# Kernel optimization log

Hardware: AMD Instinct MI355X
Metric: run time of the kernel (lower is better)

Reference implementation:

```python
import jax, jax.numpy as jnp
import numpy as np

L = 8192   # sequence length
B = 4      # batch
D = 512    # embed_dim
NDIM = 16  # EMA state dim
Z = 128    # shared q/k dim
W = 128    # attention window
MP = 256   # max relative positions
NEG = -50000.0  # TOKEN_SELF_ATTN_VALUE-style mask fill


def setup_inputs() -> dict:
    key = jax.random.key(0)
    ks = jax.random.split(key, 16)
    def tn(k, shp, std):  # truncated-normal-ish init (clipped normal)
        return jnp.clip(jax.random.normal(k, shp) * std, -2 * std, 2 * std)
    val = jnp.ones((NDIM, 1)).at[1::2].set(-1.0)  # MultiHeadEMA beta init pattern
    return {
        "x": jax.random.normal(ks[0], (L, B, D), dtype=jnp.float32),
        "delta": tn(ks[1], (D, NDIM, 1), 0.2),
        "alpha": tn(ks[2], (D, NDIM, 1), 0.2),
        "beta": tn(ks[3], (D, NDIM, 1), 0.02) + val,
        "gamma": jax.random.normal(ks[4], (D, NDIM)),
        "omega": jax.random.normal(ks[5], (D,)),
        "Wp": tn(ks[6], (D, 1), 0.02),      # LatentConfigurator weight_proj
        "bp": jnp.zeros((1,)),
        "temp": jnp.array([0.5 * np.log(D)], dtype=jnp.float32),  # log(sqrt(D))
        "Wz": tn(ks[7], (D, Z), 0.02),
        "qg": jax.random.normal(ks[8], (Z,)) * 0.02 + 1.0,
        "qb": jnp.zeros((Z,)),
        "kg": jax.random.normal(ks[9], (Z,)) * 0.02 + 1.0,
        "kb": jnp.zeros((Z,)),
        "Wv": tn(ks[10], (D, D), 0.02),
        "relb": tn(ks[11], (2 * MP - 1,), 0.02),  # FastRelativePositionalBias table
    }


def _rotary(t, cos, sin):
    # t: (B, L, Z); cos/sin: (L, Z//2). Complex rotation on interleaved pairs.
    t1, t2 = t[..., 0::2], t[..., 1::2]
    return jnp.stack([t1 * cos - t2 * sin, t1 * sin + t2 * cos], axis=-1).reshape(t.shape)


def _forward(x, delta, alpha, beta, gamma, omega, Wp, bp, temp, Wz, qg, qb, kg, kb, Wv, relb):
    scale = 1.0 / np.sqrt(NDIM)
    # ---- MultiHeadEMA: damped EMA as long convolution via FFT ----
    p = jax.nn.sigmoid(delta)                      # (D,N,1)
    a = jax.nn.sigmoid(alpha)
    logq = jnp.log1p(-(p * a))                     # log(1 - p*alpha)
    t = jnp.arange(L, dtype=jnp.float32)
    kern = (p * beta) * jnp.exp(logq * t)          # (D,N,L) Vandermonde kernel
    k1d = jnp.einsum('dnl,dn->dl', kern, gamma * scale)  # (D,L)
    xb = x.transpose(1, 2, 0)                      # (B,D,L)
    conv = jnp.fft.irfft(jnp.fft.rfft(xb, n=2 * L) * jnp.fft.rfft(k1d, n=2 * L), n=2 * L)[..., :L]
    mx = jax.nn.silu(conv.transpose(2, 0, 1) + x * omega)  # (L,B,D)
    # ---- LatentConfigurator: sigmoid token routing (proj_dim==1) ----
    pi = jax.nn.sigmoid((mx @ Wp + bp) / jnp.exp(temp))[..., 0].T  # (B,L)
    mxb = mx.transpose(1, 0, 2)                    # (B,L,D)
    sel = pi > 0.5
    idx = jnp.cumsum(sel.astype(jnp.int32), axis=1) * sel  # (B,L); 0 -> dropped slot
    counts = sel.sum(axis=1)                       # (B,)
    bi = jnp.arange(B)[:, None]
    # compress_seq: scatter selected tokens to compact prefix (slot 0 dropped)
    c = jnp.zeros((B, L + 1, D), mx.dtype).at[bi, idx].add(mxb * sel[..., None])[:, 1:]
    # ---- windowed attention over compressed tokens ----
    z = jax.nn.silu(c @ Wz)                        # (B,L,Z)
    freqs = 1.0 / (10000.0 ** (jnp.arange(0, Z, 2, dtype=jnp.float32) / Z))
    ang = jnp.arange(L, dtype=jnp.float32)[:, None] * freqs
    cos, sin = jnp.cos(ang), jnp.sin(ang)
    q = _rotary(z * qg + qb, cos, sin)
    kk = _rotary(z * kg + kb, cos, sin)
    v = jax.nn.silu(c @ Wv)                        # (B,L,D)
    n = L // W
    qw = q.reshape(B, n, W, Z)
    def look_around(tw):  # prepend previous window: (B,n,W,f) -> (B,n,2W,f)
        prev = jnp.pad(tw, ((0, 0), (1, 0), (0, 0), (0, 0)))[:, :-1]
        return jnp.concatenate([prev, tw], axis=2)
    kw = look_around(kk.reshape(B, n, W, Z))
    vw = look_around(v.reshape(B, n, W, D))
    base = (jnp.arange(n) * W)[:, None, None]
    qabs = base + jnp.arange(W)[None, :, None]         # (n,W,1)
    kabs = base + jnp.arange(-W, W)[None, None, :]     # (n,1,2W)
    mask = (kabs <= qabs) & (kabs >= 0) & (kabs[None] < counts[:, None, None, None])  # (B,n,W,2W)
    rel = jnp.arange(-W, W)[None, :] - jnp.arange(W)[:, None]   # (W,2W)
    bias = relb[jnp.clip(rel + MP - 1, 0, 2 * MP - 2)]          # (W,2W)
    scores = jnp.einsum('bnwz,bnkz->bnwk', qw, kw) / np.sqrt(Z) + bias
    attn = jax.nn.softmax(jnp.where(mask, scores, NEG), axis=-1)
    h = jnp.einsum('bnwk,bnkd->bnwd', attn, vw).reshape(B, L, D)
    # ---- extract: gather back to original positions, gate by pi ----
    hpad = jnp.concatenate([jnp.zeros((B, 1, D), h.dtype), h], axis=1)
    hsel = jnp.take_along_axis(hpad, idx[..., None], axis=1)    # (B,L,D)
    return x + (hsel * pi[..., None]).transpose(1, 0, 2)        # (L,B,D)


def reference(x, delta, alpha, beta, gamma, omega, Wp, bp, temp, Wz, qg, qb, kg, kb, Wv, relb):
    return _forward(x, delta, alpha, beta, gamma, omega, Wp, bp, temp, Wz, qg, qb, kg, kb, Wv, relb)
```

## Files before the change

### kernel.cpp

```cpp
#include <hip/hip_runtime.h>
#include <math.h>

constexpr int L = 8192;
constexpr int B = 4;
constexpr int D = 512;
constexpr int NDIM = 16;
constexpr int Z = 128;
constexpr float NEGF = -50000.0f;
constexpr int CCL = 32;
constexpr int NCH = L / CCL;
constexpr int FMAX = 64;

typedef short s16x8 __attribute__((ext_vector_type(8)));
typedef float f32x4 __attribute__((ext_vector_type(4)));

typedef __attribute__((address_space(1))) const void* as1cv;
typedef __attribute__((address_space(3))) void* as3v;

__device__ __forceinline__ void gld16(const void* g, void* l) {
  __builtin_amdgcn_global_load_lds((as1cv)g, (as3v)l, 16, 0, 0);
}

__device__ __forceinline__ unsigned short f2bf(float f) {
  unsigned u = __builtin_bit_cast(unsigned, f);
  u += 0x7fffu + ((u >> 16) & 1u);
  return (unsigned short)(u >> 16);
}

#define DPPADD(acc, ctrl, rmask)                                                   \
  {                                                                                \
    int _mv = __builtin_amdgcn_update_dpp(0, __builtin_bit_cast(int, acc),         \
                                          ctrl, rmask, 0xf, false);                \
    acc += __builtin_bit_cast(float, _mv);                                         \
  }

__global__ __launch_bounds__(256) void k_prep(const float* __restrict__ delta,
                                              const float* __restrict__ alpha,
                                              const float* __restrict__ beta,
                                              const float* __restrict__ gamma,
                                              double* __restrict__ qdn,
                                              double* __restrict__ cdn,
                                              double* __restrict__ rp1,
                                              double* __restrict__ rp2,
                                              float* __restrict__ qf,
                                              float* __restrict__ cf,
                                              float* __restrict__ r1f,
                                              float* __restrict__ r2f,
                                              float* __restrict__ r3f,
                                              int* __restrict__ fcnt) {
  int i = blockIdx.x * 256 + threadIdx.x;
  if (i == 0) *fcnt = 0;
  if (i >= D * NDIM) return;
  double p = 1.0 / (1.0 + exp(-(double)delta[i]));
  double a = 1.0 / (1.0 + exp(-(double)alpha[i]));
  double q = 1.0 - p * a;
  double c = p * (double)beta[i] * (double)gamma[i] * 0.25;
  qdn[i] = q; cdn[i] = c;
  double q2 = q * q, q4 = q2 * q2, q8 = q4 * q4;
  double q16 = q8 * q8, q32 = q16 * q16, q64 = q32 * q32;
  rp1[i] = q64;
  rp2[i] = q64 * q64;
  qf[i] = (float)q; cf[i] = (float)c;
  r1f[i] = (float)q32;
  r2f[i] = (float)q64;
  r3f[i] = (float)(q64 * q32);
}

__global__ __launch_bounds__(256) void k_tab(float2* __restrict__ tab) {
  int tid = blockIdx.x * 256 + threadIdx.x;
  int i = tid & 63, j = tid >> 6;
  float freq = __expf(((float)(-2 * i) / 128.0f) * 9.210340371976184f);
  float angf = (float)j * freq;
  float sa, ca;
  __sincosf(angf, &sa, &ca);
  float2 r; r.x = ca; r.y = sa;
  tab[tid] = r;
}

__global__ __launch_bounds__(256, 4) void k_convA(const float* __restrict__ x,
                                                  const float* __restrict__ qf,
                                                  float* __restrict__ E) {
  int bx = blockIdx.x;
  int tile = bx & 63, dg = (bx >> 6) & 7, b = bx >> 9;
  int dl = threadIdx.x & 63, cl = threadIdx.x >> 6;
  int dgl = dg * 64 + dl;
  int t = tile * 4 + cl;
  float q[NDIM], s[NDIM];
#pragma unroll
  for (int n = 0; n < NDIM; ++n) { q[n] = qf[dgl * NDIM + n]; s[n] = 0.f; }
  const float* xp = x + ((size_t)(t * CCL) * B + b) * D + dgl;
  float xv[CCL];
#pragma unroll
  for (int u = 0; u < CCL; ++u) xv[u] = xp[u * (B * D)];
#pragma unroll
  for (int u = 0; u < CCL; ++u) {
#pragma unroll
    for (int n = 0; n < NDIM; ++n) s[n] = fmaf(q[n], s[n], xv[u]);
  }
  float* eb = E + ((size_t)(b * NCH + t) * NDIM) * 512 + dgl;
#pragma unroll
  for (int n = 0; n < NDIM; ++n) eb[(size_t)n * 512] = s[n];
}

__global__ __launch_bounds__(256, 4) void k_convC(const float* __restrict__ x,
                                                  const float* __restrict__ omega,
                                                  const float* __restrict__ qf,
                                                  const float* __restrict__ cf,
                                                  const float* __restrict__ r1f,
                                                  const float* __restrict__ r2f,
                                                  const float* __restrict__ r3f,
                                                  const float* __restrict__ E,
                                                  const float* __restrict__ Wp,
                                                  unsigned short* __restrict__ mxb,
                                                  float* __restrict__ pdot) {
  int bx = blockIdx.x;
  int tile = bx & 63, dg = (bx >> 6) & 7, b = bx >> 9;
  int dl = threadIdx.x & 63, cl = threadIdx.x >> 6;
  int dgl = dg * 64 + dl;
  int t = tile * 4 + cl;
  float q[NDIM], c[NDIM], s[NDIM];
#pragma unroll
  for (int n = 0; n < NDIM; ++n) {
    q[n] = qf[dgl * NDIM + n];
    c[n] = cf[dgl * NDIM + n];
    s[n] = 0.f;
  }
  if (t >= 1) {
    const float* e1 = E + ((size_t)(b * NCH + t - 1) * NDIM) * 512 + dgl;
#pragma unroll
    for (int n = 0; n < NDIM; ++n) s[n] = e1[(size_t)n * 512];
  }
  if (t >= 2) {
    const float* e2 = E + ((size_t)(b * NCH + t - 2) * NDIM) * 512 + dgl;
#pragma unroll
    for (int n = 0; n < NDIM; ++n) s[n] = fmaf(r1f[dgl * NDIM + n], e2[(size_t)n * 512], s[n]);
  }
  if (t >= 3) {
    const float* e3 = E + ((size_t)(b * NCH + t - 3) * NDIM) * 512 + dgl;
#pragma unroll
    for (int n = 0; n < NDIM; ++n) s[n] = fmaf(r2f[dgl * NDIM + n], e3[(size_t)n * 512], s[n]);
  }
  if (t >= 4) {
    const float* e4 = E + ((size_t)(b * NCH + t - 4) * NDIM) * 512 + dgl;
#pragma unroll
    for (int n = 0; n < NDIM; ++n) s[n] = fmaf(r3f[dgl * NDIM + n], e4[(size_t)n * 512], s[n]);
  }
  float om = omega[dgl];
  float wp = Wp[dgl];
  const float* xp = x + ((size_t)(t * CCL) * B + b) * D + dgl;
  unsigned short* mp = mxb + ((size_t)b * L + t * CCL) * 512 + dgl;
  float* pp = pdot + ((size_t)(b * L + t * CCL)) * 8 + dg;
  float xv[CCL];
#pragma unroll
  for (int u = 0; u < CCL; ++u) xv[u] = xp[u * (B * D)];
#pragma unroll
  for (int u = 0; u < CCL; ++u) {
#pragma unroll
    for (int n = 0; n < NDIM; ++n) s[n] = fmaf(q[n], s[n], xv[u]);
    float p0 = c[0] * s[0], p1 = c[1] * s[1], p2 = c[2] * s[2], p3 = c[3] * s[3];
    p0 = fmaf(c[4], s[4], p0);  p1 = fmaf(c[5], s[5], p1);
    p2 = fmaf(c[6], s[6], p2);  p3 = fmaf(c[7], s[7], p3);
    p0 = fmaf(c[8], s[8], p0);  p1 = fmaf(c[9], s[9], p1);
    p2 = fmaf(c[10], s[10], p2); p3 = fmaf(c[11], s[11], p3);
    p0 = fmaf(c[12], s[12], p0); p1 = fmaf(c[13], s[13], p1);
    p2 = fmaf(c[14], s[14], p2); p3 = fmaf(c[15], s[15], p3);
    float conv = (p0 + p1) + (p2 + p3);
    float m = fmaf(xv[u], om, conv);
    float v = m / (1.0f + __expf(-m));
    mp[(size_t)u * 512] = f2bf(v);
    float pd = v * wp;
    DPPADD(pd, 0x111, 0xf);
    DPPADD(pd, 0x112, 0xf);
    DPPADD(pd, 0x114, 0xf);
    DPPADD(pd, 0x118, 0xf);
    DPPADD(pd, 0x142, 0xa);
    DPPADD(pd, 0x143, 0x8);
    if (dl == 63) pp[(size_t)u * 8] = pd;
  }
}

__global__ __launch_bounds__(256) void k_logitc(const float* __restrict__ pdot,
                                                const float* __restrict__ bp,
                                                const float* __restrict__ temp,
                                                float* __restrict__ pi,
                                                int* __restrict__ selb,
                                                int* __restrict__ fcnt,
                                                int* __restrict__ flags) {
  int rid = blockIdx.x * 256 + threadIdx.x;
  const float* pr = pdot + (size_t)rid * 8;
  double acc = 0.0;
#pragma unroll
  for (int j = 0; j < 8; ++j) acc += (double)pr[j];
  double logit = acc + (double)bp[0];
  pi[rid] = (float)(1.0 / (1.0 + exp(-logit / exp((double)temp[0]))));
  selb[rid] = (logit > 0.0) ? 1 : 0;
  if (fabs(logit) < 1e-4) {
    int slot = atomicAdd(fcnt, 1);
    if (slot < FMAX) flags[slot] = rid;
  }
}

__global__ __launch_bounds__(256) void k_fix(const int* __restrict__ fcnt,
                                             const int* __restrict__ flags,
                                             const float* __restrict__ x,
                                             const double* __restrict__ qdn,
                                             const double* __restrict__ cdn,
                                             const double* __restrict__ rp1,
                                             const double* __restrict__ rp2,
                                             const float* __restrict__ omega,
                                             const float* __restrict__ Wp,
                                             double* __restrict__ pfix) {
  int nb = blockIdx.x;
  int fi = nb >> 3, dblk = nb & 7;
  int count = *fcnt; if (count > FMAX) count = FMAX;
  if (fi >= count) return;
  int rid = flags[fi];
  int b = rid >> 13, l = rid & (L - 1);
  int t = l >> 6, io = l & 63;
  int sub = threadIdx.x >> 6, dl = threadIdx.x & 63;
  int d = dblk * 64 + dl;
  double q[NDIM], s[NDIM];
#pragma unroll
  for (int n = 0; n < NDIM; ++n) { q[n] = qdn[d * NDIM + n]; s[n] = 0.0; }
  int c0 = (sub < 3) ? (t - 3 + sub) : t;
  int steps = (sub < 3) ? 64 : (io + 1);
  if (c0 >= 0) {
    const float* xp = x + ((size_t)(c0 * 64) * B + b) * D + d;
    for (int i = 0; i < steps; ++i) {
      double xv = (double)xp[(size_t)i * (B * D)];
#pragma unroll
      for (int n = 0; n < NDIM; ++n) s[n] = fma(q[n], s[n], xv);
    }
  }
  __shared__ double Esm[4][64][NDIM];
#pragma unroll
  for (int n = 0; n < NDIM; ++n) Esm[sub][dl][n] = s[n];
  __syncthreads();
  if (sub == 3) {
    double sfin[NDIM];
#pragma unroll
    for (int n = 0; n < NDIM; ++n) {
      double base = q[n], r = 1.0;
      int e = io + 1;
      while (e) { if (e & 1) r *= base; base *= base; e >>= 1; }
      double S = Esm[2][dl][n] + rp1[d * NDIM + n] * Esm[1][dl][n] + rp2[d * NDIM + n] * Esm[0][dl][n];
      sfin[n] = Esm[3][dl][n] + r * S;
    }
    double conv = 0.0;
#pragma unroll
    for (int n = 0; n < NDIM; ++n) conv = fma(cdn[d * NDIM + n], sfin[n], conv);
    double xv = (double)x[((size_t)l * B + b) * D + d];
    double m = conv + xv * (double)omega[d];
    double mxd = m / (1.0 + exp(-m));
    double v = mxd * (double)Wp[d];
#pragma unroll
    for (int off = 32; off; off >>= 1) v += __shfl_down(v, off, 64);
    if (dl == 0) pfix[fi * 8 + dblk] = v;
  }
}

__global__ __launch_bounds__(64) void k_fix2(const int* __restrict__ fcnt,
                                             const int* __restrict__ flags,
                                             const double* __restrict__ pfix,
                                             const float* __restrict__ bp,
                                             const float* __restrict__ temp,
                                             float* __restrict__ pi,
                                             int* __restrict__ selb) {
  int fi = threadIdx.x;
  int count = *fcnt; if (count > FMAX) count = FMAX;
  if (fi >= count) return;
  double s = 0.0;
#pragma unroll
  for (int j = 0; j < 8; ++j) s += pfix[fi * 8 + j];
  double logit = s + (double)bp[0];
  int rid = flags[fi];
  selb[rid] = (logit > 0.0) ? 1 : 0;
  pi[rid] = (float)(1.0 / (1.0 + exp(-logit / exp((double)temp[0]))));
}

__global__ __launch_bounds__(256) void k_scan(const int* __restrict__ selb,
                                              int* __restrict__ idx,
                                              int* __restrict__ src,
                                              int* __restrict__ counts) {
  int b = blockIdx.x;
  int t = threadIdx.x;
  __shared__ int part[256];
  const int PER = L / 256;
  int base = b * L + t * PER;
  int loc[PER];
  int cnt = 0;
#pragma unroll
  for (int i = 0; i < PER; ++i) { loc[i] = selb[base + i]; cnt += loc[i]; }
  part[t] = cnt;
  __syncthreads();
  for (int off = 1; off < 256; off <<= 1) {
    int v = (t >= off) ? part[t - off] : 0;
    __syncthreads();
    part[t] += v;
    __syncthreads();
  }
  int run = (t == 0) ? 0 : part[t - 1];
#pragma unroll
  for (int i = 0; i < PER; ++i) {
    int sflag = loc[i];
    run += sflag;
    idx[base + i] = sflag ? run : 0;
    if (sflag) src[b * L + run - 1] = t * PER + i;
  }
  if (t == 255) counts[b] = part[255];
  __syncthreads();
  int total = part[255];
  for (int i2 = total + t; i2 < L; i2 += 256) src[b * L + i2] = 0;
}

__global__ __launch_bounds__(256) void k_wt(const float* __restrict__ Wm,
                                            unsigned short* __restrict__ Wt, int N) {
  int idx = blockIdx.x * 256 + threadIdx.x;
  int n = idx >> 9, kk = idx & 511;
  Wt[idx] = f2bf(Wm[(size_t)kk * N + n]);
}

__global__ __launch_bounds__(256) void k_gemm_mfma(const unsigned short* __restrict__ mxb,
                                                   const int* __restrict__ src,
                                                   const int* __restrict__ counts,
                                                   const unsigned short* __restrict__ Bt,
                                                   float* __restrict__ outF,
                                                   unsigned short* __restrict__ outT,
                                                   int N, int mode) {
  __shared__ char smem[32768];
  char* As = smem;
  char* Bs = smem + 16384;
  int tid = threadIdx.x;
  int w = tid >> 6, l = tid & 63;
  int mtile, ntile;
  if (mode == 1) {
    int lin = blockIdx.y * 256 + blockIdx.x;
    int xcd = lin & 7, loc = lin >> 3;
    mtile = xcd * 32 + (loc >> 2);
    ntile = loc & 3;
  } else {
    mtile = blockIdx.x; ntile = blockIdx.y;
  }
  int m0 = mtile * 128, n0 = ntile * 128;
  int gb = m0 >> 13, j0 = m0 & 8191;
  if (j0 >= counts[gb]) return;
  int wr = w >> 1, wc = w & 1;
  const unsigned short* arow[4];
  const unsigned short* brow[4];
#pragma unroll
  for (int ld = 0; ld < 4; ++ld) {
    int li = w * 4 + ld;
    int row = li * 8 + (l >> 3);
    int col = ((l & 7) ^ (row & 7)) << 3;
    int srow = src[gb * 8192 + j0 + row];
    arow[ld] = mxb + ((size_t)gb * 8192 + srow) * 512 + col;
    brow[ld] = Bt + (size_t)(n0 + row) * 512 + col;
  }
  f32x4 acc[4][4];
  f32x4 zz = {0.f, 0.f, 0.f, 0.f};
#pragma unroll
  for (int mi = 0; mi < 4; ++mi)
#pragma unroll
    for (int ni = 0; ni < 4; ++ni) acc[mi][ni] = zz;

  for (int k0 = 0; k0 < 512; k0 += 64) {
#pragma unroll
    for (int ld = 0; ld < 4; ++ld) {
      int li = w * 4 + ld;
      gld16(arow[ld] + k0, As + li * 1024);
      gld16(brow[ld] + k0, Bs + li * 1024);
    }
    __syncthreads();
    s16x8 af[4][2], bfr[4][2];
#pragma unroll
    for (int kh = 0; kh < 2; ++kh) {
#pragma unroll
      for (int mi = 0; mi < 4; ++mi) {
        int row = wr * 64 + mi * 16 + (l & 15);
        int byte = row * 128 + ((kh * 64 + ((l >> 4) * 16)) ^ ((row & 7) << 4));
        af[mi][kh] = *(const s16x8*)(As + byte);
      }
#pragma unroll
      for (int ni = 0; ni < 4; ++ni) {
        int row = wc * 64 + ni * 16 + (l & 15);
        int byte = row * 128 + ((kh * 64 + ((l >> 4) * 16)) ^ ((row & 7) << 4));
        bfr[ni][kh] = *(const s16x8*)(Bs + byte);
      }
    }
#pragma unroll
    for (int kh = 0; kh < 2; ++kh)
#pragma unroll
      for (int mi = 0; mi < 4; ++mi)
#pragma unroll
        for (int ni = 0; ni < 4; ++ni)
          acc[mi][ni] = __builtin_amdgcn_mfma_f32_16x16x32_bf16(af[mi][kh], bfr[ni][kh], acc[mi][ni], 0, 0, 0);
    __syncthreads();
  }
  if (mode == 0) {
#pragma unroll
    for (int mi = 0; mi < 4; ++mi)
#pragma unroll
      for (int ni = 0; ni < 4; ++ni)
#pragma unroll
        for (int r = 0; r < 4; ++r) {
          float vv = acc[mi][ni][r];
          vv = vv / (1.0f + __expf(-vv));
          int mrow = m0 + wr * 64 + mi * 16 + (l >> 4) * 4 + r;
          int ncol = n0 + wc * 64 + ni * 16 + (l & 15);
          outF[(size_t)mrow * N + ncol] = vv;
        }
  } else {
#pragma unroll
    for (int mi = 0; mi < 4; ++mi)
#pragma unroll
      for (int ni = 0; ni < 4; ++ni)
#pragma unroll
        for (int r = 0; r < 4; ++r) {
          float vv = acc[mi][ni][r];
          vv = vv / (1.0f + __expf(-vv));
          int mrow = wr * 64 + mi * 16 + (l >> 4) * 4 + r;
          int ncol = wc * 64 + ni * 16 + (l & 15);
          int byteoff = ncol * 256 + ((mrow * 2) ^ ((ncol & 7) << 4));
          *(unsigned short*)(smem + byteoff) = f2bf(vv);
        }
    __syncthreads();
#pragma unroll
    for (int it = 0; it < 8; ++it) {
      int ncol = w * 32 + it * 4 + (l >> 4);
      int ch = l & 15;
      int byteoff = ncol * 256 + ((ch * 16) ^ ((ncol & 7) << 4));
      s16x8 vch = *(const s16x8*)(smem + byteoff);
      *(s16x8*)(outT + ((size_t)(gb * 512 + n0 + ncol)) * 8192 + j0 + ch * 8) = vch;
    }
  }
}

__global__ __launch_bounds__(256) void k_rot(const float* __restrict__ z,
                                             const float2* __restrict__ tab,
                                             const int* __restrict__ counts,
                                             const float* __restrict__ qg,
                                             const float* __restrict__ qb,
                                             const float* __restrict__ kg,
                                             const float* __restrict__ kb,
                                             unsigned short* __restrict__ qo,
                                             unsigned short* __restrict__ ko) {
  int tid = blockIdx.x * 256 + threadIdx.x;
  int i = tid & 63;
  int row = tid >> 6;
  int j = row & (L - 1);
  int b = row >> 13;
  if (j >= counts[b]) return;
  float2 cs = tab[j * 64 + i];
  float cc = cs.x, ss = cs.y;
  size_t base = (size_t)row * Z + 2 * i;
  float z1 = z[base], z2 = z[base + 1];
  float q1 = z1 * qg[2 * i] + qb[2 * i], q2 = z2 * qg[2 * i + 1] + qb[2 * i + 1];
  float k1 = z1 * kg[2 * i] + kb[2 * i], k2 = z2 * kg[2 * i + 1] + kb[2 * i + 1];
  qo[base]     = f2bf(q1 * cc - q2 * ss);
  qo[base + 1] = f2bf(q1 * ss + q2 * cc);
  ko[base]     = f2bf(k1 * cc - k2 * ss);
  ko[base + 1] = f2bf(k1 * ss + k2 * cc);
}

__global__ __launch_bounds__(256) void k_attn_mfma(const unsigned short* __restrict__ q,
                                                   const unsigned short* __restrict__ k,
                                                   const unsigned short* __restrict__ vT,
                                                   const float* __restrict__ relb,
                                                   const int* __restrict__ counts,
                                                   const int* __restrict__ src,
                                                   const float* __restrict__ pi,
                                                   const float* __restrict__ x,
                                                   float* __restrict__ out) {
  __shared__ char smem[49152];
  char* A  = smem;
  char* Bv = smem + 32768;
  int tid = threadIdx.x, w = tid >> 6, l = tid & 63;
  int bid = blockIdx.x;
  int n = bid >> 3, b = (bid >> 1) & 3, half = bid & 1;
  int cnt = counts[b];
  int q0 = n * 128 + half * 64;
  if (q0 >= cnt) return;
  int kbase = n * 128 - 128;
  const size_t rowb = (size_t)b * L;
  int m0 = w * 16;
  int lg = l >> 4;

  s16x8 aq[4];
  {
    const unsigned short* qrow = q + (rowb + q0 + m0 + (l & 15)) * Z + lg * 8;
#pragma unroll
    for (int ks = 0; ks < 4; ++ks) aq[ks] = *(const s16x8*)(qrow + ks * 32);
  }

  f32x4 s[16];
  f32x4 zz = {0.f, 0.f, 0.f, 0.f};
#pragma unroll
  for (int ni = 0; ni < 16; ++ni) s[ni] = zz;
#pragma unroll
  for (int kh2 = 0; kh2 < 2; ++kh2) {
#pragma unroll
    for (int ld = 0; ld < 8; ++ld) {
      int li = w * 8 + ld;
      int rowl = li * 4 + (l >> 4);
      int jk = kbase + kh2 * 128 + rowl;
      if (jk < 0) jk = 0;
      int colb = ((l & 15) * 16) ^ ((rowl & 7) << 4);
      gld16((const char*)(k + (rowb + jk) * Z) + colb, A + li * 1024);
    }
    __syncthreads();
#pragma unroll
    for (int ni8 = 0; ni8 < 8; ++ni8) {
      int ni = kh2 * 8 + ni8;
      int rowl = ni8 * 16 + (l & 15);
      int rb = rowl * 256, sw = (rowl & 7) << 4;
#pragma unroll
      for (int ks = 0; ks < 4; ++ks) {
        s16x8 bk = *(const s16x8*)(A + rb + ((ks * 64 + lg * 16) ^ sw));
        s[ni] = __builtin_amdgcn_mfma_f32_16x16x32_bf16(aq[ks], bk, s[ni], 0, 0, 0);
      }
    }
    __syncthreads();
  }

  auto stageV = [&](int nc) {
#pragma unroll
    for (int ld = 0; ld < 4; ++ld) {
      int li = w * 4 + ld;
      int row = li * 2 + (l >> 5);
      int colb = ((l & 31) * 16) ^ ((row & 7) << 4);
      int j = kbase + (colb >> 1);
      if (j < 0) j = 0;
      gld16((const char*)(vT + ((size_t)(b * 512 + nc * 32 + row)) * L + j), Bv + li * 1024);
    }
  };
  stageV(0);

  int rgrp = lg * 4;
  float mxr[4] = {-3e38f, -3e38f, -3e38f, -3e38f};
#pragma unroll
  for (int ni = 0; ni < 16; ++ni) {
    int col = ni * 16 + (l & 15);
    int kabs = kbase + col;
#pragma unroll
    for (int r = 0; r < 4; ++r) {
      int ww = half * 64 + m0 + rgrp + r;
      bool valid = (kabs >= 0) && (kabs <= n * 128 + ww) && (kabs < cnt);
      float vv = valid ? (s[ni][r] * 0.08838834764831845f + relb[col + 127 - ww]) : NEGF;
      s[ni][r] = vv;
      mxr[r] = fmaxf(mxr[r], vv);
    }
  }
#pragma unroll
  for (int r = 0; r < 4; ++r)
    for (int off = 1; off < 16; off <<= 1)
      mxr[r] = fmaxf(mxr[r], __shfl_xor(mxr[r], off, 64));
  float smr[4] = {0.f, 0.f, 0.f, 0.f};
#pragma unroll
  for (int ni = 0; ni < 16; ++ni)
#pragma unroll
    for (int r = 0; r < 4; ++r) {
      float p = __expf(s[ni][r] - mxr[r]);
      s[ni][r] = p;
      smr[r] += p;
    }
#pragma unroll
  for (int r = 0; r < 4; ++r) {
    for (int off = 1; off < 16; off <<= 1) smr[r] += __shfl_xor(smr[r], off, 64);
    smr[r] = 1.0f / smr[r];
  }
#pragma unroll
  for (int ni = 0; ni < 16; ++ni) {
    int colb2 = (ni * 16 + (l & 15)) * 2;
#pragma unroll
    for (int r = 0; r < 4; ++r) {
      int row = m0 + rgrp + r;
      *(unsigned short*)(A + row * 512 + (colb2 ^ ((row & 7) << 4))) = f2bf(s[ni][r] * smr[r]);
    }
  }
  __syncthreads();

  s16x8 pa[8];
  {
    int prow = m0 + (l & 15);
    int psw = (prow & 7) << 4;
#pragma unroll
    for (int kt = 0; kt < 8; ++kt)
      pa[kt] = *(const s16x8*)(A + prow * 512 + ((kt * 64 + lg * 16) ^ psw));
  }

  int tlr[4]; float pvr[4]; bool vr[4];
#pragma unroll
  for (int r = 0; r < 4; ++r) {
    int jq = q0 + m0 + rgrp + r;
    vr[r] = (jq < cnt);
    int tl = vr[r] ? src[(b << 13) + jq] : 0;
    tlr[r] = tl;
    pvr[r] = pi[(b << 13) + tl];
  }

  for (int nc = 0; nc < 16; ++nc) {
    if (nc) {
      __syncthreads();
      stageV(nc);
      __syncthreads();
    }
    f32x4 o[2];
#pragma unroll
    for (int ni = 0; ni < 2; ++ni) o[ni] = zz;
#pragma unroll
    for (int kt = 0; kt < 4; ++kt) {
      s16x8 pa0 = pa[kt * 2];
      s16x8 pa1 = pa[kt * 2 + 1];
#pragma unroll
      for (int ni = 0; ni < 2; ++ni) {
        int vrow = ni * 16 + (l & 15);
        int vsw = (vrow & 7) << 4;
        s16x8 vb0 = *(const s16x8*)(Bv + vrow * 512 + ((kt * 128 + lg * 16) ^ vsw));
        s16x8 vb1 = *(const s16x8*)(Bv + vrow * 512 + ((kt * 128 + 64 + lg * 16) ^ vsw));
        o[ni] = __builtin_amdgcn_mfma_f32_16x16x32_bf16(pa0, vb0, o[ni], 0, 0, 0);
        o[ni] = __builtin_amdgcn_mfma_f32_16x16x32_bf16(pa1, vb1, o[ni], 0, 0, 0);
      }
    }
#pragma unroll
    for (int ni = 0; ni < 2; ++ni)
#pragma unroll
      for (int r = 0; r < 4; ++r)
        if (vr[r]) {
          size_t off = ((size_t)tlr[r] * B + b) * 512 + nc * 32 + ni * 16 + (l & 15);
          out[off] = fmaf(o[ni][r], pvr[r], x[off]);
        }
  }
}

__global__ __launch_bounds__(256) void k_fill(const float* __restrict__ x,
                                              const int* __restrict__ idx,
                                              float* __restrict__ out) {
  int e4 = blockIdx.x * 256 + threadIdx.x;
  int rem = e4 >> 7;
  int b = rem & 3;
  int l = rem >> 2;
  if (idx[(b << 13) + l] == 0)
    ((float4*)out)[e4] = ((const float4*)x)[e4];
}

extern "C" void kernel_launch(void* const* d_in, const int* in_sizes, int n_in,
                              void* d_out, int out_size, void* d_ws, size_t ws_size,
                              hipStream_t stream) {
  const float* x     = (const float*)d_in[0];
  const float* delta = (const float*)d_in[1];
  const float* alpha = (const float*)d_in[2];
  const float* beta  = (const float*)d_in[3];
  const float* gamma = (const float*)d_in[4];
  const float* omega = (const float*)d_in[5];
  const float* Wp    = (const float*)d_in[6];
  const float* bp    = (const float*)d_in[7];
  const float* temp  = (const float*)d_in[8];
  const float* Wz    = (const float*)d_in[9];
  const float* qg    = (const float*)d_in[10];
  const float* qb    = (const float*)d_in[11];
  const float* kg    = (const float*)d_in[12];
  const float* kb    = (const float*)d_in[13];
  const float* Wv    = (const float*)d_in[14];
  const float* relb  = (const float*)d_in[15];
  (void)in_sizes; (void)n_in; (void)out_size; (void)ws_size;

  char* wsb = (char*)d_ws;
  size_t o = 0;
  auto alloc = [&](size_t bytes) {
    char* p = wsb + o;
    o += (bytes + 255) & ~(size_t)255;
    return p;
  };
  unsigned short* mxb  = (unsigned short*)alloc((size_t)B * L * D * 2);
  float* Ebuf          = (float*)alloc((size_t)B * NCH * NDIM * 512 * 4);
  float* zb            = (float*)alloc((size_t)B * L * Z * 4);
  unsigned short* qb2  = (unsigned short*)alloc((size_t)B * L * Z * 2);
  unsigned short* kb2  = (unsigned short*)alloc((size_t)B * L * Z * 2);
  unsigned short* vTb  = (unsigned short*)alloc((size_t)B * D * L * 2);
  unsigned short* wzt  = (unsigned short*)alloc((size_t)Z * 512 * 2);
  unsigned short* wvt  = (unsigned short*)alloc((size_t)D * 512 * 2);
  float2* tab = (float2*)alloc((size_t)L * 64 * 8);
  float* pdot = (float*)alloc((size_t)B * L * 8 * 4);
  float* pib  = (float*)alloc((size_t)B * L * 4);
  int* selb   = (int*)alloc((size_t)B * L * 4);
  int* idx    = (int*)alloc((size_t)B * L * 4);
  int* src    = (int*)alloc((size_t)B * L * 4);
  int* cnt    = (int*)alloc(256);
  double* qdn = (double*)alloc((size_t)D * NDIM * 8);
  double* cdn = (double*)alloc((size_t)D * NDIM * 8);
  double* rp1 = (double*)alloc((size_t)D * NDIM * 8);
  double* rp2 = (double*)alloc((size_t)D * NDIM * 8);
  float* qf   = (float*)alloc((size_t)D * NDIM * 4);
  float* cf   = (float*)alloc((size_t)D * NDIM * 4);
  float* r1f  = (float*)alloc((size_t)D * NDIM * 4);
  float* r2f  = (float*)alloc((size_t)D * NDIM * 4);
  float* r3f  = (float*)alloc((size_t)D * NDIM * 4);
  int* fcnt   = (int*)alloc(256);
  int* flags  = (int*)alloc(FMAX * 4);
  double* pfix = (double*)alloc((size_t)FMAX * 8 * 8);

  k_prep<<<(D * NDIM + 255) / 256, 256, 0, stream>>>(delta, alpha, beta, gamma,
                                                     qdn, cdn, rp1, rp2, qf, cf, r1f, r2f, r3f, fcnt);
  k_tab<<<L * 64 / 256, 256, 0, stream>>>(tab);
  k_convA<<<B * 8 * 64, 256, 0, stream>>>(x, qf, Ebuf);
  k_convC<<<B * 8 * 64, 256, 0, stream>>>(x, omega, qf, cf, r1f, r2f, r3f, Ebuf, Wp, mxb, pdot);
  k_logitc<<<B * L / 256, 256, 0, stream>>>(pdot, bp, temp, pib, selb, fcnt, flags);
  k_fix<<<FMAX * 8, 256, 0, stream>>>(fcnt, flags, x, qdn, cdn, rp1, rp2, omega, Wp, pfix);
  k_fix2<<<1, 64, 0, stream>>>(fcnt, flags, pfix, bp, temp, pib, selb);
  k_scan<<<B, 256, 0, stream>>>(selb, idx, src, cnt);
  k_wt<<<Z * 512 / 256, 256, 0, stream>>>(Wz, wzt, Z);
  k_wt<<<D * 512 / 256, 256, 0, stream>>>(Wv, wvt, D);
  k_gemm_mfma<<<dim3(256, 1), 256, 0, stream>>>(mxb, src, cnt, wzt, zb, vTb, Z, 0);
  k_gemm_mfma<<<dim3(256, 4), 256, 0, stream>>>(mxb, src, cnt, wvt, zb, vTb, D, 1);
  k_rot<<<B * L * (Z / 2) / 256, 256, 0, stream>>>(zb, tab, cnt, qg, qb, kg, kb, qb2, kb2);
  k_fill<<<(int)((size_t)L * B * D / 4 / 256), 256, 0, stream>>>(x, idx, (float*)d_out);
  k_attn_mfma<<<512, 256, 0, stream>>>(qb2, kb2, vTb, relb, cnt, src, pib, x, (float*)d_out);
}
```

Before: 230.0 us.

## Double-buffer K and V LDS staging in attention kernel to overlap loads

The attention kernel now stages K in four 64-row chunks and V per 32-column slice into alternating LDS buffers. It prefetches the next chunk while running MFMAs on the current one, and the first K and V tiles are issued before the Q register loads. This is meant to hide global-to-LDS load latency and remove one barrier per V iteration. The cost is raising shared memory from 48KB to 64KB per block, which may lower the number of resident blocks per CU.

```diff
diff --git a/kernel.cpp b/kernel.cpp
--- a/kernel.cpp
+++ b/kernel.cpp
@@ -471,7 +471,7 @@
                                                    const float* __restrict__ pi,
                                                    const float* __restrict__ x,
                                                    float* __restrict__ out) {
-  __shared__ char smem[49152];
+  __shared__ char smem[65536];
   char* A  = smem;
   char* Bv = smem + 32768;
   int tid = threadIdx.x, w = tid >> 6, l = tid & 63;
@@ -485,44 +485,18 @@
   int m0 = w * 16;
   int lg = l >> 4;
 
-  s16x8 aq[4];
-  {
-    const unsigned short* qrow = q + (rowb + q0 + m0 + (l & 15)) * Z + lg * 8;
-#pragma unroll
-    for (int ks = 0; ks < 4; ++ks) aq[ks] = *(const s16x8*)(qrow + ks * 32);
-  }
-
-  f32x4 s[16];
-  f32x4 zz = {0.f, 0.f, 0.f, 0.f};
-#pragma unroll
-  for (int ni = 0; ni < 16; ++ni) s[ni] = zz;
-#pragma unroll
-  for (int kh2 = 0; kh2 < 2; ++kh2) {
-#pragma unroll
-    for (int ld = 0; ld < 8; ++ld) {
-      int li = w * 8 + ld;
+  auto stageK = [&](int qi, char* buf) {
+#pragma unroll
+    for (int ld = 0; ld < 4; ++ld) {
+      int li = w * 4 + ld;
       int rowl = li * 4 + (l >> 4);
-      int jk = kbase + kh2 * 128 + rowl;
+      int jk = kbase + qi * 64 + rowl;
       if (jk < 0) jk = 0;
       int colb = ((l & 15) * 16) ^ ((rowl & 7) << 4);
-      gld16((const char*)(k + (rowb + jk) * Z) + colb, A + li * 1024);
-    }
-    __syncthreads();
-#pragma unroll
-    for (int ni8 = 0; ni8 < 8; ++ni8) {
-      int ni = kh2 * 8 + ni8;
-      int rowl = ni8 * 16 + (l & 15);
-      int rb = rowl * 256, sw = (rowl & 7) << 4;
-#pragma unroll
-      for (int ks = 0; ks < 4; ++ks) {
-        s16x8 bk = *(const s16x8*)(A + rb + ((ks * 64 + lg * 16) ^ sw));
-        s[ni] = __builtin_amdgcn_mfma_f32_16x16x32_bf16(aq[ks], bk, s[ni], 0, 0, 0);
-      }
-    }
-    __syncthreads();
-  }
-
-  auto stageV = [&](int nc) {
+      gld16((const char*)(k + (rowb + jk) * Z) + colb, buf + li * 1024);
+    }
+  };
+  auto stageV = [&](int nc, char* buf) {
 #pragma unroll
     for (int ld = 0; ld < 4; ++ld) {
       int li = w * 4 + ld;
@@ -530,10 +504,42 @@
       int colb = ((l & 31) * 16) ^ ((row & 7) << 4);
       int j = kbase + (colb >> 1);
       if (j < 0) j = 0;
-      gld16((const char*)(vT + ((size_t)(b * 512 + nc * 32 + row)) * L + j), Bv + li * 1024);
+      gld16((const char*)(vT + ((size_t)(b * 512 + nc * 32 + row)) * L + j), buf + li * 1024);
     }
   };
-  stageV(0);
+
+  stageK(0, A);
+  stageV(0, Bv);
+
+  s16x8 aq[4];
+  {
+    const unsigned short* qrow = q + (rowb + q0 + m0 + (l & 15)) * Z + lg * 8;
+#pragma unroll
+    for (int ks = 0; ks < 4; ++ks) aq[ks] = *(const s16x8*)(qrow + ks * 32);
+  }
+
+  f32x4 s[16];
+  f32x4 zz = {0.f, 0.f, 0.f, 0.f};
+#pragma unroll
+  for (int ni = 0; ni < 16; ++ni) s[ni] = zz;
+#pragma unroll
+  for (int qi = 0; qi < 4; ++qi) {
+    char* cur = A + (qi & 1) * 16384;
+    __syncthreads();
+    if (qi < 3) stageK(qi + 1, A + ((qi + 1) & 1) * 16384);
+#pragma unroll
+    for (int ni4 = 0; ni4 < 4; ++ni4) {
+      int ni = qi * 4 + ni4;
+      int rowl = ni4 * 16 + (l & 15);
+      int rb = rowl * 256, sw = (rowl & 7) << 4;
+#pragma unroll
+      for (int ks = 0; ks < 4; ++ks) {
+        s16x8 bk = *(const s16x8*)(cur + rb + ((ks * 64 + lg * 16) ^ sw));
+        s[ni] = __builtin_amdgcn_mfma_f32_16x16x32_bf16(aq[ks], bk, s[ni], 0, 0, 0);
+      }
+    }
+  }
+  __syncthreads();
 
   int rgrp = lg * 4;
   float mxr[4] = {-3e38f, -3e38f, -3e38f, -3e38f};
@@ -599,11 +605,9 @@
   }
 
   for (int nc = 0; nc < 16; ++nc) {
-    if (nc) {
-      __syncthreads();
-      stageV(nc);
-      __syncthreads();
-    }
+    char* cur = Bv + (nc & 1) * 16384;
+    if (nc) __syncthreads();
+    if (nc < 15) stageV(nc + 1, Bv + ((nc + 1) & 1) * 16384);
     f32x4 o[2];
 #pragma unroll
     for (int ni = 0; ni < 2; ++ni) o[ni] = zz;
@@ -615,8 +619,8 @@
       for (int ni = 0; ni < 2; ++ni) {
         int vrow = ni * 16 + (l & 15);
         int vsw = (vrow & 7) << 4;
-        s16x8 vb0 = *(const s16x8*)(Bv + vrow * 512 + ((kt * 128 + lg * 16) ^ vsw));
-        s16x8 vb1 = *(const s16x8*)(Bv + vrow * 512 + ((kt * 128 + 64 + lg * 16) ^ vsw));
+        s16x8 vb0 = *(const s16x8*)(cur + vrow * 512 + ((kt * 128 + lg * 16) ^ vsw));
+        s16x8 vb1 = *(const s16x8*)(cur + vrow * 512 + ((kt * 128 + 64 + lg * 16) ^ vsw));
         o[ni] = __builtin_amdgcn_mfma_f32_16x16x32_bf16(pa0, vb0, o[ni], 0, 0, 0);
         o[ni] = __builtin_amdgcn_mfma_f32_16x16x32_bf16(pa1, vb1, o[ni], 0, 0, 0);
       }
```

New measurement: 227.5 us. About the same (-1.1%).
